# Kernel tuning notes

Measured on AMD Instinct MI355X. Metric: run time of the kernel, lower is better.

The kernel has to match this reference:

```python
import jax, jax.numpy as jnp
import numpy as np

EPSILON = 1e-08

def setup_inputs() -> dict:
    key0 = jax.random.key(0)
    kq, kk, kv = jax.random.split(key0, 3)
    B, Q, H, D = 64, 16, 1, 64
    KV, DV = 16384, 64
    query = jax.random.normal(kq, (B, Q, H, D), dtype=jnp.float32)
    key = jax.random.normal(kk, (B, KV, H, D), dtype=jnp.float32)
    value = jax.random.normal(kv, (B, KV, H, DV), dtype=jnp.float32)
    return {"query": query, "key": key, "value": value}

def reference(query, key, value):
    # InvertedDotProductAttention(norm_type='mean', multi_head=False)
    d = query.shape[-1]
    q = query / jnp.sqrt(jnp.asarray(d, dtype=query.dtype))
    # logits: [b, h, q, k]
    attn = jnp.einsum('bqhd,bkhd->bhqk', q, key)
    # inverted attention: softmax over the query axis (-2)
    attn = jax.nn.softmax(attn, axis=-2)
    # renormalize_keys=True (norm_type == 'mean'): normalize over key axis
    attn = attn / (jnp.sum(attn, axis=-1, keepdims=True) + EPSILON)
    out = jnp.einsum('bhqk,bkhd->bqhd', attn, value)
    # multi_head=False -> squeeze the (singleton) heads axis
    return jnp.squeeze(out, axis=-2)
```

## Files before the change

### kernel.cpp

```cpp
#include <hip/hip_runtime.h>

namespace {

typedef float f32x4 __attribute__((ext_vector_type(4)));
typedef short bf16x8 __attribute__((ext_vector_type(8)));

constexpr int Bn = 64, QN = 16, Dn = 64, DVn = 64, KVn = 16384;
constexpr int SPLITS  = 8;
constexpr int TILE    = 64;
constexpr int THREADS = 256;
constexpr int NT      = KVn / (SPLITS * TILE);
constexpr int AP      = 68;

constexpr float SCALE = 0.125f * 1.4426950408889634f;

__device__ __forceinline__ unsigned cvt_pk_bf16(float a, float b) {
    unsigned r;
    asm("v_cvt_pk_bf16_f32 %0, %1, %2" : "=v"(r) : "v"(a), "v"(b));
    return r;
}

union FragU { unsigned u[4]; bf16x8 v; };

__device__ __forceinline__ void split8(const float* x, bf16x8& hi, bf16x8& lo) {
    FragU uh, ul;
#pragma unroll
    for (int p = 0; p < 4; ++p) {
        const float a = x[2 * p], b2 = x[2 * p + 1];
        const unsigned h = cvt_pk_bf16(a, b2);
        uh.u[p] = h;
        const float ha = __uint_as_float(h << 16);
        const float hb = __uint_as_float(h & 0xffff0000u);
        ul.u[p] = cvt_pk_bf16(a - ha, b2 - hb);
    }
    hi = uh.v; lo = ul.v;
}

__device__ __forceinline__ void gl_lds16(const float* g, float* l) {
    __builtin_amdgcn_global_load_lds(
        (const __attribute__((address_space(1))) unsigned int*)g,
        (__attribute__((address_space(3))) unsigned int*)l,
        16, 0, 0);
}

__global__ __launch_bounds__(THREADS, 2)
void inv_attn_part(const float* __restrict__ query,
                   const float* __restrict__ key,
                   const float* __restrict__ value,
                   float* __restrict__ pout,
                   float* __restrict__ pden)
{
    __shared__ __align__(16) float kbuf[2][TILE * Dn];
    __shared__ __align__(16) float vbuf[2][TILE * DVn];
    __shared__ __align__(16) float a_s[2][QN * AP];
    __shared__ float den_buf[4][QN];

    const int tid  = threadIdx.x;
    const int lane = tid & 63;
    const int w    = tid >> 6;
    const int l15  = lane & 15;
    const int g    = lane >> 4;
    const int spl  = blockIdx.x;
    const int b    = blockIdx.y;
    const int kt0  = spl * NT * TILE;

    bf16x8 qhi[2], qlo[2];
    {
        const float* qp = query + ((size_t)b * QN + l15) * Dn + g * 8;
#pragma unroll
        for (int ks = 0; ks < 2; ++ks) {
            const float4 u0 = *reinterpret_cast<const float4*>(qp + ks * 32);
            const float4 u1 = *reinterpret_cast<const float4*>(qp + ks * 32 + 4);
            float x[8] = {u0.x * SCALE, u0.y * SCALE, u0.z * SCALE, u0.w * SCALE,
                          u1.x * SCALE, u1.y * SCALE, u1.z * SCALE, u1.w * SCALE};
            split8(x, qhi[ks], qlo[ks]);
        }
    }

    f32x4 oacc = {0.f, 0.f, 0.f, 0.f};
    float den0 = 0.f, den1 = 0.f, den2 = 0.f, den3 = 0.f;

    const int srow   = lane >> 4;
    const int schunk = lane & 15;
    const float* kg = key   + ((size_t)b * KVn + kt0) * Dn;
    const float* vg = value + ((size_t)b * KVn + kt0) * Dn;

    auto issue_tile = [&](int t, int buf) {
#pragma unroll
        for (int i = 0; i < 4; ++i) {
            const int r  = w * 16 + i * 4 + srow;
            const int sc = schunk ^ (r & 7);
            const size_t off = (size_t)(t * TILE + r) * Dn + sc * 4;
            gl_lds16(kg + off, &kbuf[buf][(w * 16 + i * 4) * Dn]);
            gl_lds16(vg + off, &vbuf[buf][(w * 16 + i * 4) * DVn]);
        }
    };

    issue_tile(0, 0);

    for (int t = 0; t < NT; ++t) {
        const int buf = t & 1;

        __syncthreads();

        if (t + 1 < NT) issue_tile(t + 1, buf ^ 1);

        const int rq = w * 16 + l15;
        const int sw = rq & 7;
        f32x4 sacc = {0.f, 0.f, 0.f, 0.f};
#pragma unroll
        for (int ks = 0; ks < 2; ++ks) {
            const int c0 = ks * 8 + g * 2;
            const f32x4 r0 = *reinterpret_cast<const f32x4*>(
                &kbuf[buf][rq * Dn + ((c0    ) ^ sw) * 4]);
            const f32x4 r1 = *reinterpret_cast<const f32x4*>(
                &kbuf[buf][rq * Dn + ((c0 + 1) ^ sw) * 4]);
            float x[8] = {r0[0], r0[1], r0[2], r0[3], r1[0], r1[1], r1[2], r1[3]};
            bf16x8 khi, klo;
            split8(x, khi, klo);
            sacc = __builtin_amdgcn_mfma_f32_16x16x32_bf16(qhi[ks], khi, sacc, 0, 0, 0);
            sacc = __builtin_amdgcn_mfma_f32_16x16x32_bf16(qhi[ks], klo, sacc, 0, 0, 0);
            sacc = __builtin_amdgcn_mfma_f32_16x16x32_bf16(qlo[ks], khi, sacc, 0, 0, 0);
        }

        float m = fmaxf(fmaxf(sacc[0], sacc[1]), fmaxf(sacc[2], sacc[3]));
        m = fmaxf(m, __shfl_xor(m, 16, 64));
        m = fmaxf(m, __shfl_xor(m, 32, 64));
        float p0 = exp2f(sacc[0] - m), p1 = exp2f(sacc[1] - m);
        float p2 = exp2f(sacc[2] - m), p3 = exp2f(sacc[3] - m);
        float s4 = p0 + p1 + p2 + p3;
        s4 += __shfl_xor(s4, 16, 64);
        s4 += __shfl_xor(s4, 32, 64);
        const float inv = 1.0f / s4;
        p0 *= inv; p1 *= inv; p2 *= inv; p3 *= inv;
        a_s[buf][(g * 4 + 0) * AP + rq] = p0;
        a_s[buf][(g * 4 + 1) * AP + rq] = p1;
        a_s[buf][(g * 4 + 2) * AP + rq] = p2;
        a_s[buf][(g * 4 + 3) * AP + rq] = p3;
        den0 += p0; den1 += p1; den2 += p2; den3 += p3;

        __syncthreads();

        const int dv = w * 16 + l15;
        const int ch = dv >> 2, wrd = dv & 3;
#pragma unroll
        for (int ks = 0; ks < 2; ++ks) {
            const int base = ks * 32 + g * 8;
            const float4 a0 = *reinterpret_cast<const float4*>(&a_s[buf][l15 * AP + base]);
            const float4 a1 = *reinterpret_cast<const float4*>(&a_s[buf][l15 * AP + base + 4]);
            FragU ua;
            ua.u[0] = cvt_pk_bf16(a0.x, a0.y);
            ua.u[1] = cvt_pk_bf16(a0.z, a0.w);
            ua.u[2] = cvt_pk_bf16(a1.x, a1.y);
            ua.u[3] = cvt_pk_bf16(a1.z, a1.w);
            float vx[8];
#pragma unroll
            for (int j = 0; j < 8; ++j) {
                const int k = base + j;
                vx[j] = vbuf[buf][k * DVn + ((ch ^ j) << 2) + wrd];
            }
            FragU uv;
            uv.u[0] = cvt_pk_bf16(vx[0], vx[1]);
            uv.u[1] = cvt_pk_bf16(vx[2], vx[3]);
            uv.u[2] = cvt_pk_bf16(vx[4], vx[5]);
            uv.u[3] = cvt_pk_bf16(vx[6], vx[7]);
            oacc = __builtin_amdgcn_mfma_f32_16x16x32_bf16(ua.v, uv.v, oacc, 0, 0, 0);
        }
    }

    const size_t obase = (((size_t)b * SPLITS + spl) * QN) * DVn;
    const int dvo = w * 16 + l15;
    pout[obase + (g * 4 + 0) * DVn + dvo] = oacc[0];
    pout[obase + (g * 4 + 1) * DVn + dvo] = oacc[1];
    pout[obase + (g * 4 + 2) * DVn + dvo] = oacc[2];
    pout[obase + (g * 4 + 3) * DVn + dvo] = oacc[3];

#pragma unroll
    for (int off = 1; off < 16; off <<= 1) {
        den0 += __shfl_xor(den0, off, 64);
        den1 += __shfl_xor(den1, off, 64);
        den2 += __shfl_xor(den2, off, 64);
        den3 += __shfl_xor(den3, off, 64);
    }
    if (l15 == 0) {
        den_buf[w][g * 4 + 0] = den0;
        den_buf[w][g * 4 + 1] = den1;
        den_buf[w][g * 4 + 2] = den2;
        den_buf[w][g * 4 + 3] = den3;
    }
    __syncthreads();
    if (tid < QN) {
        const float d = den_buf[0][tid] + den_buf[1][tid] + den_buf[2][tid] + den_buf[3][tid];
        pden[((size_t)b * SPLITS + spl) * QN + tid] = d;
    }
}

__global__ __launch_bounds__(256)
void inv_attn_reduce(const float* __restrict__ pout,
                     const float* __restrict__ pden,
                     float* __restrict__ out)
{
    const int gid = blockIdx.x * blockDim.x + threadIdx.x;
    const int dv = gid & 63;
    const int q  = (gid >> 6) & (QN - 1);
    const int b  = gid >> 10;
    float sum = 0.f, den = 0.f;
#pragma unroll 8
    for (int sp = 0; sp < SPLITS; ++sp) {
        sum += pout[(((size_t)b * SPLITS + sp) * QN + q) * DVn + dv];
        den += pden[((size_t)b * SPLITS + sp) * QN + q];
    }
    out[gid] = sum / (den + 1e-8f);
}

}

extern "C" void kernel_launch(void* const* d_in, const int* in_sizes, int n_in,
                              void* d_out, int out_size, void* d_ws, size_t ws_size,
                              hipStream_t stream) {
    const float* query = (const float*)d_in[0];
    const float* key   = (const float*)d_in[1];
    const float* value = (const float*)d_in[2];
    float* out = (float*)d_out;

    float* pout = (float*)d_ws;
    float* pden = pout + (size_t)Bn * SPLITS * QN * DVn;

    dim3 grid1(SPLITS, Bn);
    inv_attn_part<<<grid1, THREADS, 0, stream>>>(query, key, value, pout, pden);

    const int total = Bn * QN * DVn;
    inv_attn_reduce<<<total / 256, 256, 0, stream>>>(pout, pden, out);
}
```

Baseline: 102.3 us.

## Deepen K/V prefetch to three LDS slots and halve KV splits

Replaces the double-buffered K/V staging with a three-slot ring that prefetches two tiles ahead. Synchronisation now uses explicit vmcnt/lgkmcnt waits plus raw barriers, and the softmax scratch buffer becomes a single copy. KV splits drop from 8 to 4 and launch bounds allow one block per CU, so each block walks a longer run of keys and the reduce pass has less partial data to combine. The aim is more memory-level parallelism per block and fewer partial results, at the cost of half the blocks and lower wave occupancy, which may leave latency less hidden.

```diff
diff --git a/kernel.cpp b/kernel.cpp
--- a/kernel.cpp
+++ b/kernel.cpp
@@ -6,10 +6,11 @@
 typedef short bf16x8 __attribute__((ext_vector_type(8)));
 
 constexpr int Bn = 64, QN = 16, Dn = 64, DVn = 64, KVn = 16384;
-constexpr int SPLITS  = 8;
+constexpr int SPLITS  = 4;
 constexpr int TILE    = 64;
 constexpr int THREADS = 256;
 constexpr int NT      = KVn / (SPLITS * TILE);
+constexpr int NSLOT   = 3;
 constexpr int AP      = 68;
 
 constexpr float SCALE = 0.125f * 1.4426950408889634f;
@@ -43,16 +44,16 @@
         16, 0, 0);
 }
 
-__global__ __launch_bounds__(THREADS, 2)
+__global__ __launch_bounds__(THREADS, 1)
 void inv_attn_part(const float* __restrict__ query,
                    const float* __restrict__ key,
                    const float* __restrict__ value,
                    float* __restrict__ pout,
                    float* __restrict__ pden)
 {
-    __shared__ __align__(16) float kbuf[2][TILE * Dn];
-    __shared__ __align__(16) float vbuf[2][TILE * DVn];
-    __shared__ __align__(16) float a_s[2][QN * AP];
+    __shared__ __align__(16) float kbuf[NSLOT][TILE * Dn];
+    __shared__ __align__(16) float vbuf[NSLOT][TILE * DVn];
+    __shared__ __align__(16) float a_s[QN * AP];
     __shared__ float den_buf[4][QN];
 
     const int tid  = threadIdx.x;
@@ -85,25 +86,29 @@
     const float* kg = key   + ((size_t)b * KVn + kt0) * Dn;
     const float* vg = value + ((size_t)b * KVn + kt0) * Dn;
 
-    auto issue_tile = [&](int t, int buf) {
+    auto issue_tile = [&](int t, int slot) {
 #pragma unroll
         for (int i = 0; i < 4; ++i) {
             const int r  = w * 16 + i * 4 + srow;
             const int sc = schunk ^ (r & 7);
             const size_t off = (size_t)(t * TILE + r) * Dn + sc * 4;
-            gl_lds16(kg + off, &kbuf[buf][(w * 16 + i * 4) * Dn]);
-            gl_lds16(vg + off, &vbuf[buf][(w * 16 + i * 4) * DVn]);
+            gl_lds16(kg + off, &kbuf[slot][(w * 16 + i * 4) * Dn]);
+            gl_lds16(vg + off, &vbuf[slot][(w * 16 + i * 4) * DVn]);
         }
     };
 
     issue_tile(0, 0);
+    issue_tile(1, 1);
 
     for (int t = 0; t < NT; ++t) {
-        const int buf = t & 1;
-
-        __syncthreads();
-
-        if (t + 1 < NT) issue_tile(t + 1, buf ^ 1);
+        const int slot = t % NSLOT;
+
+        if (t + 1 < NT) asm volatile("s_waitcnt vmcnt(8)" ::: "memory");
+        else            asm volatile("s_waitcnt vmcnt(0)" ::: "memory");
+        __builtin_amdgcn_s_barrier();
+        __builtin_amdgcn_sched_barrier(0);
+
+        if (t + 2 < NT) issue_tile(t + 2, (t + 2) % NSLOT);
 
         const int rq = w * 16 + l15;
         const int sw = rq & 7;
@@ -112,9 +117,9 @@
         for (int ks = 0; ks < 2; ++ks) {
             const int c0 = ks * 8 + g * 2;
             const f32x4 r0 = *reinterpret_cast<const f32x4*>(
-                &kbuf[buf][rq * Dn + ((c0    ) ^ sw) * 4]);
+                &kbuf[slot][rq * Dn + ((c0    ) ^ sw) * 4]);
             const f32x4 r1 = *reinterpret_cast<const f32x4*>(
-                &kbuf[buf][rq * Dn + ((c0 + 1) ^ sw) * 4]);
+                &kbuf[slot][rq * Dn + ((c0 + 1) ^ sw) * 4]);
             float x[8] = {r0[0], r0[1], r0[2], r0[3], r1[0], r1[1], r1[2], r1[3]};
             bf16x8 khi, klo;
             split8(x, khi, klo);
@@ -133,21 +138,23 @@
         s4 += __shfl_xor(s4, 32, 64);
         const float inv = 1.0f / s4;
         p0 *= inv; p1 *= inv; p2 *= inv; p3 *= inv;
-        a_s[buf][(g * 4 + 0) * AP + rq] = p0;
-        a_s[buf][(g * 4 + 1) * AP + rq] = p1;
-        a_s[buf][(g * 4 + 2) * AP + rq] = p2;
-        a_s[buf][(g * 4 + 3) * AP + rq] = p3;
+        a_s[(g * 4 + 0) * AP + rq] = p0;
+        a_s[(g * 4 + 1) * AP + rq] = p1;
+        a_s[(g * 4 + 2) * AP + rq] = p2;
+        a_s[(g * 4 + 3) * AP + rq] = p3;
         den0 += p0; den1 += p1; den2 += p2; den3 += p3;
 
-        __syncthreads();
+        asm volatile("s_waitcnt lgkmcnt(0)" ::: "memory");
+        __builtin_amdgcn_s_barrier();
+        __builtin_amdgcn_sched_barrier(0);
 
         const int dv = w * 16 + l15;
         const int ch = dv >> 2, wrd = dv & 3;
 #pragma unroll
         for (int ks = 0; ks < 2; ++ks) {
             const int base = ks * 32 + g * 8;
-            const float4 a0 = *reinterpret_cast<const float4*>(&a_s[buf][l15 * AP + base]);
-            const float4 a1 = *reinterpret_cast<const float4*>(&a_s[buf][l15 * AP + base + 4]);
+            const float4 a0 = *reinterpret_cast<const float4*>(&a_s[l15 * AP + base]);
+            const float4 a1 = *reinterpret_cast<const float4*>(&a_s[l15 * AP + base + 4]);
             FragU ua;
             ua.u[0] = cvt_pk_bf16(a0.x, a0.y);
             ua.u[1] = cvt_pk_bf16(a0.z, a0.w);
@@ -157,7 +164,7 @@
 #pragma unroll
             for (int j = 0; j < 8; ++j) {
                 const int k = base + j;
-                vx[j] = vbuf[buf][k * DVn + ((ch ^ j) << 2) + wrd];
+                vx[j] = vbuf[slot][k * DVn + ((ch ^ j) << 2) + wrd];
             }
             FragU uv;
             uv.u[0] = cvt_pk_bf16(vx[0], vx[1]);
@@ -205,7 +212,7 @@
     const int q  = (gid >> 6) & (QN - 1);
     const int b  = gid >> 10;
     float sum = 0.f, den = 0.f;
-#pragma unroll 8
+#pragma unroll
     for (int sp = 0; sp < SPLITS; ++sp) {
         sum += pout[(((size_t)b * SPLITS + sp) * QN + q) * DVn + dv];
         den += pden[((size_t)b * SPLITS + sp) * QN + q];
```

Result: slower. 137.0 us (+33.9%).
